# Kernel tuning notes

Hardware: AMD Instinct MI355X
Metric: run time of the kernel (lower is better)

Reference implementation:

```python
import jax, jax.numpy as jnp
import numpy as np

N, K, A, P, HID = 32768, 32, 4, 128, 256
RELMAX, NBINS, DMIN, DMAX = 32, 16, 0.0, 22.0
EPS = 1e-6


def _frames(pos):
    # Gram-Schmidt rigid frame from backbone atoms N(0), CA(1), C(2).
    v1 = pos[:, 2] - pos[:, 1]
    v2 = pos[:, 0] - pos[:, 1]
    e1 = v1 / (jnp.linalg.norm(v1, axis=-1, keepdims=True) + EPS)
    u2 = v2 - jnp.sum(v2 * e1, axis=-1, keepdims=True) * e1
    e2 = u2 / (jnp.linalg.norm(u2, axis=-1, keepdims=True) + EPS)
    e3 = jnp.cross(e1, e2)
    R = jnp.stack([e1, e2, e3], axis=-1)  # [N,3,3], columns are basis vectors
    t = pos[:, 1]                         # CA translation
    return R, t


def _rbf(d):
    centers = jnp.linspace(DMIN, DMAX, NBINS)
    sigma = (DMAX - DMIN) / NBINS
    return jnp.exp(-((d[..., None] - centers) ** 2) / (2.0 * sigma ** 2))


def setup_inputs() -> dict:
    key = jax.random.key(0)
    ks = jax.random.split(key, 12)
    g = lambda k, shape: jax.random.normal(k, shape) / jnp.sqrt(jnp.float32(shape[0]))
    return {
        "pos": jax.random.normal(ks[0], (N, A, 3)) * 3.0,
        "neighbours": jax.random.randint(ks[1], (N, K), 0, N),
        "resi": jnp.arange(N),
        "chain": jnp.zeros((N,), jnp.int32),
        "batch": jnp.zeros((N,), jnp.int32),
        "mask": jnp.ones((N,), jnp.float32),
        "W_rel": g(ks[2], (2 * RELMAX + 1, P)),
        "W_dist": g(ks[3], (NBINS, P)),
        "W_dir": g(ks[4], (3, P)),
        "W_rot": g(ks[5], (9, P)),
        "W_vec": g(ks[6], (A * 3, P)),
        "ln_scale": jnp.ones((P,), jnp.float32),
        "ln_bias": jnp.zeros((P,), jnp.float32),
        "W1": g(ks[7], (P, HID)),
        "b1": jnp.zeros((HID,), jnp.float32),
        "W2": g(ks[8], (HID, P)),
        "b2": jnp.zeros((P,), jnp.float32),
    }


def reference(pos, neighbours, resi, chain, batch, mask,
              W_rel, W_dist, W_dir, W_rot, W_vec,
              ln_scale, ln_bias, W1, b1, W2, b2):
    # pair mask: both residues valid and neighbour not padded
    pair_mask = mask[:, None] * mask[neighbours] * (neighbours != -1)

    # --- sequence relative position (one-hot, clipped, same chain/batch) ---
    same = ((chain[:, None] == chain[neighbours]) &
            (batch[:, None] == batch[neighbours]))
    rel = jnp.clip(resi[neighbours] - resi[:, None], -RELMAX, RELMAX) + RELMAX
    rel_oh = jax.nn.one_hot(rel, 2 * RELMAX + 1, dtype=pos.dtype) * same[..., None]
    pair = jnp.einsum("nkf,fp->nkp", rel_oh, W_rel)

    # --- distance features (CA-CA RBF) ---
    ca = pos[:, 1]                                      # [N,3]
    diff = ca[neighbours] - ca[:, None]                 # [N,K,3]
    d = jnp.sqrt(jnp.sum(diff * diff, axis=-1) + EPS)
    pair += jnp.einsum("nkf,fp->nkp", _rbf(d), W_dist)

    # --- direction features (unit vector in local frame of i) ---
    R, t = _frames(pos)
    unit = diff / (d[..., None] + EPS)
    local_dir = jnp.einsum("nab,nka->nkb", R, unit)     # R_i^T u
    pair += jnp.einsum("nkf,fp->nkp", local_dir, W_dir)

    # --- relative rotation features R_i^T R_j, flattened ---
    Rj = R[neighbours]                                  # [N,K,3,3]
    rel_rot = jnp.einsum("nab,nkac->nkbc", R, Rj).reshape(pos.shape[0], K, 9)
    pair += jnp.einsum("nkf,fp->nkp", rel_rot, W_rot)

    # --- pair vector features: neighbour atoms in frame of i ---
    vec = pos[neighbours] - t[:, None, None]            # [N,K,A,3]
    local_vec = jnp.einsum("nab,nkAa->nkAb", R, vec).reshape(pos.shape[0], K, A * 3)
    pair += jnp.einsum("nkf,fp->nkp", local_vec, W_vec)

    # --- LayerNorm over feature dim ---
    mu = jnp.mean(pair, axis=-1, keepdims=True)
    var = jnp.mean((pair - mu) ** 2, axis=-1, keepdims=True)
    pair = (pair - mu) / jnp.sqrt(var + 1e-5) * ln_scale + ln_bias

    # --- MLP (gelu, hidden = 2 * pair_size) ---
    h = jax.nn.gelu(jnp.einsum("nkp,ph->nkh", pair, W1) + b1)
    pair = jnp.einsum("nkh,hp->nkp", h, W2) + b2
    return pair, pair_mask


if __name__ == "__main__":
    out, pm = reference(**setup_inputs())
    print(out.shape, pm.shape)
```

## Files before the change

### kernel.cpp

```cpp
#include <hip/hip_runtime.h>
#include <hip/hip_bf16.h>

#define N_NODES 32768
#define NK      1048576

typedef __bf16 bf16x8 __attribute__((ext_vector_type(8)));
typedef float  f32x4  __attribute__((ext_vector_type(4)));
typedef short  short4v __attribute__((ext_vector_type(4)));
typedef int    int4v  __attribute__((ext_vector_type(4)));
typedef int    int2v  __attribute__((ext_vector_type(2)));

#define WAIT_LGKM() asm volatile("s_waitcnt lgkmcnt(0)" ::: "memory")

static __device__ __forceinline__ unsigned fbits(float f) {
    union { float f; unsigned u; } v; v.f = f; return v.u;
}
static __device__ __forceinline__ unsigned short f2bf(float f) {
    unsigned u = fbits(f);
    return (unsigned short)((u + 0x7fffu + ((u >> 16) & 1u)) >> 16);
}

static __device__ __forceinline__ void make_frame(const float* __restrict__ p, float* __restrict__ R) {
    float v1x = p[6]-p[3], v1y = p[7]-p[4], v1z = p[8]-p[5];
    float v2x = p[0]-p[3], v2y = p[1]-p[4], v2z = p[2]-p[5];
    float i1 = 1.f/(sqrtf(v1x*v1x+v1y*v1y+v1z*v1z)+1e-6f);
    float e1x=v1x*i1, e1y=v1y*i1, e1z=v1z*i1;
    float dt = v2x*e1x+v2y*e1y+v2z*e1z;
    float u2x=v2x-dt*e1x, u2y=v2y-dt*e1y, u2z=v2z-dt*e1z;
    float i2 = 1.f/(sqrtf(u2x*u2x+u2y*u2y+u2z*u2z)+1e-6f);
    float e2x=u2x*i2, e2y=u2y*i2, e2z=u2z*i2;
    float e3x = e1y*e2z - e1z*e2y;
    float e3y = e1z*e2x - e1x*e2z;
    float e3z = e1x*e2y - e1y*e2x;
    R[0]=e1x; R[1]=e2x; R[2]=e3x;
    R[3]=e1y; R[4]=e2y; R[5]=e3y;
    R[6]=e1z; R[7]=e2z; R[8]=e3z;
}

__global__ void sd_prep_weights(const float* __restrict__ W1, const float* __restrict__ W2,
                                const float* __restrict__ Wd, const float* __restrict__ Wdir,
                                const float* __restrict__ Wrot, const float* __restrict__ Wvec,
                                unsigned short* __restrict__ wftp, unsigned short* __restrict__ w1p,
                                unsigned short* __restrict__ w2p) {
    int i = blockIdx.x*256 + threadIdx.x;
    if (i < 8192) {
        int fragid = i >> 9, lane = (i >> 3) & 63, j = i & 7;
        int pb = fragid >> 1, ks = fragid & 1;
        int f = 8*(lane>>4) + j + 32*ks;
        int p = pb*16 + (lane & 15);
        float v = 0.f;
        if (f < 16)       v = Wd[f*128+p];
        else if (f < 19)  v = Wdir[(f-16)*128+p];
        else if (f < 28)  v = Wrot[(f-19)*128+p];
        else if (f < 40)  v = Wvec[(f-28)*128+p];
        wftp[i] = f2bf(v);
    } else if (i < 40960) {
        int idx = i - 8192;
        int fragid = idx >> 9, lane = (idx >> 3) & 63, j = idx & 7;
        int ht = fragid >> 2, ks = fragid & 3;
        int h = ht*16 + (lane & 15);
        int p = 8*(lane>>4) + j + 32*ks;
        w1p[idx] = f2bf(W1[p*256 + h]);
    } else if (i < 73728) {
        int idx = i - 40960;
        int fragid = idx >> 9, lane = (idx >> 3) & 63, j = idx & 7;
        int pt = fragid >> 3, ktp = fragid & 7;
        int half = j >> 2, jj = j & 3;
        int h = (2*ktp + half)*16 + 4*(lane>>4) + jj;
        int p = pt*16 + (lane & 15);
        w2p[idx] = f2bf(W2[h*128 + p]);
    }
}

__global__ void sd_mask_kernel(const int* __restrict__ nbr, const float* __restrict__ mask,
                               float* __restrict__ outm) {
    int g = blockIdx.x*256 + threadIdx.x;
    if (g >= NK) return;
    int j = nbr[g];
    int n = g >> 5;
    float pm = mask[n] * mask[j & (N_NODES-1)] * ((j != -1) ? 1.f : 0.f);
    outm[g] = pm;
}

#define MFMA32(a,b,c) __builtin_amdgcn_mfma_f32_16x16x32_bf16((a),(b),(c),0,0,0)
#define MFMA16(a,b,c) __builtin_amdgcn_mfma_f32_16x16x16bf16_1k((a),(b),(c),0,0,0)

__global__ __launch_bounds__(256, 3) void sd_fused_kernel(
    const float* __restrict__ pos, const int* __restrict__ nbr,
    const int* __restrict__ resi, const int* __restrict__ chain,
    const int* __restrict__ batch, const float* __restrict__ W_rel,
    const float* __restrict__ ln_scale, const float* __restrict__ ln_bias,
    const float* __restrict__ b1, const float* __restrict__ b2,
    const char* __restrict__ wftp_c, const char* __restrict__ w1p_c,
    const char* __restrict__ w2p_c,
    float* __restrict__ out)
{
    __shared__ __align__(16) char smem[49664];
    const int t    = threadIdx.x;
    const int lane = t & 63;
    const int wid  = t >> 6;
    const int lrow = lane & 15;
    const int lk   = lane >> 4;
    const int edge0 = blockIdx.x * 128 + wid * 32;
    char* Fv = smem + wid * 12288;
    char* Xv = Fv + 4096;
    int* meta = (int*)(smem + 49152 + wid*128);

    {
        int4v z = (int4v){0,0,0,0};
        #pragma unroll
        for (int k = 0; k < 4; ++k) *(int4v*)(Fv + lane*64 + k*16) = z;
    }
    WAIT_LGKM();

    {
        const int e   = lane >> 1;
        const int sub = lane & 1;
        const int g   = edge0 + e;
        const int n   = g >> 5;
        const int jn  = nbr[g] & (N_NODES - 1);
        float pn[12], pj[12];
        #pragma unroll
        for (int r = 0; r < 3; ++r) {
            f32x4 a = *(const f32x4*)(pos + n*12 + r*4);
            f32x4 b = *(const f32x4*)(pos + jn*12 + r*4);
            #pragma unroll
            for (int c = 0; c < 4; ++c) { pn[r*4+c] = a[c]; pj[r*4+c] = b[c]; }
        }
        float Rn[9], Rj[9];
        make_frame(pn, Rn); make_frame(pj, Rj);
        float dx = pj[3]-pn[3], dy = pj[4]-pn[4], dz = pj[5]-pn[5];
        float d = sqrtf(dx*dx + dy*dy + dz*dz + 1e-6f);
        float inv = 1.f/(d + 1e-6f);
        float ux = dx*inv, uy = dy*inv, uz = dz*inv;
        float feats[40];
        #pragma unroll
        for (int bb = 0; bb < 16; ++bb) {
            float ee = d - (22.f/15.f)*bb;
            feats[bb] = __expf(-ee*ee*0.264462809917f);
        }
        #pragma unroll
        for (int bb = 0; bb < 3; ++bb)
            feats[16+bb] = Rn[bb]*ux + Rn[3+bb]*uy + Rn[6+bb]*uz;
        #pragma unroll
        for (int bb = 0; bb < 3; ++bb)
            #pragma unroll
            for (int cc = 0; cc < 3; ++cc)
                feats[19+bb*3+cc] = Rn[bb]*Rj[cc] + Rn[3+bb]*Rj[3+cc] + Rn[6+bb]*Rj[6+cc];
        #pragma unroll
        for (int aa = 0; aa < 4; ++aa) {
            float vx = pj[aa*3+0]-pn[3], vy = pj[aa*3+1]-pn[4], vz = pj[aa*3+2]-pn[5];
            #pragma unroll
            for (int bb = 0; bb < 3; ++bb)
                feats[28+aa*3+bb] = Rn[bb]*vx + Rn[3+bb]*vy + Rn[6+bb]*vz;
        }
        char* fb = Fv + e*128;
        const int rx = (e & 7) << 4;
        if (!sub) {
            #pragma unroll
            for (int f = 0; f < 20; ++f)
                *(unsigned short*)(fb + ((2*f) ^ rx)) = f2bf(feats[f]);
        } else {
            #pragma unroll
            for (int f = 20; f < 40; ++f)
                *(unsigned short*)(fb + ((2*f) ^ rx)) = f2bf(feats[f]);
            int same = (chain[n]==chain[jn]) & (batch[n]==batch[jn]);
            int rel = resi[jn] - resi[n];
            rel = (rel < -32 ? -32 : (rel > 32 ? 32 : rel)) + 32;
            meta[e] = same ? (rel + 1) : 0;
        }
    }
    WAIT_LGKM();

    const int rxl = (lrow & 7) << 4;

    f32x4 accF[2][8];
    #pragma unroll
    for (int ni = 0; ni < 2; ++ni)
        #pragma unroll
        for (int pb = 0; pb < 8; ++pb) accF[ni][pb] = (f32x4){0.f,0.f,0.f,0.f};
    #pragma unroll
    for (int ks = 0; ks < 2; ++ks) {
        bf16x8 a0 = *(const bf16x8*)(Fv + lrow*128       + ((16*lk + 64*ks) ^ rxl));
        bf16x8 a1 = *(const bf16x8*)(Fv + (16+lrow)*128  + ((16*lk + 64*ks) ^ rxl));
        #pragma unroll
        for (int pb = 0; pb < 8; ++pb) {
            bf16x8 b = *(const bf16x8*)(wftp_c + ((pb*2 + ks)*64 + lane)*16);
            accF[0][pb] = MFMA32(a0, b, accF[0][pb]);
            accF[1][pb] = MFMA32(a1, b, accF[1][pb]);
        }
    }

    {
        float lnSv[8], lnBv[8];
        #pragma unroll
        for (int pb = 0; pb < 8; ++pb) {
            lnSv[pb] = ln_scale[pb*16 + lrow];
            lnBv[pb] = ln_bias [pb*16 + lrow];
        }
        #pragma unroll
        for (int ni = 0; ni < 2; ++ni) {
            #pragma unroll
            for (int i = 0; i < 4; ++i) {
                int er = ni*16 + 4*lk + i;
                int mt = meta[er];
                const float* wrel = W_rel + (mt > 0 ? (mt-1)*128 : 0);
                float sv = (mt > 0) ? 1.f : 0.f;
                float s = 0.f, ss = 0.f;
                #pragma unroll
                for (int pb = 0; pb < 8; ++pb) {
                    float x = accF[ni][pb][i] + sv * wrel[pb*16 + lrow];
                    accF[ni][pb][i] = x;
                    s += x; ss += x*x;
                }
                s  += __shfl_xor(s,1);  s  += __shfl_xor(s,2);  s  += __shfl_xor(s,4);  s  += __shfl_xor(s,8);
                ss += __shfl_xor(ss,1); ss += __shfl_xor(ss,2); ss += __shfl_xor(ss,4); ss += __shfl_xor(ss,8);
                float mu  = s * 0.0078125f;
                float var = ss * 0.0078125f - mu*mu;
                float rstd = rsqrtf(var + 1e-5f);
                char* xb = Xv + er*256;
                const int rx2 = (er & 7) << 4;
                #pragma unroll
                for (int pb = 0; pb < 8; ++pb) {
                    float xv = (accF[ni][pb][i] - mu) * rstd * lnSv[pb] + lnBv[pb];
                    *(unsigned short*)(xb + ((2*(pb*16 + lrow)) ^ rx2)) = f2bf(xv);
                }
            }
        }
    }
    WAIT_LGKM();

    bf16x8 bx[2][4];
    #pragma unroll
    for (int ni = 0; ni < 2; ++ni)
        #pragma unroll
        for (int ks = 0; ks < 4; ++ks)
            bx[ni][ks] = *(const bf16x8*)(Xv + (ni*16+lrow)*256 + ((16*lk + 64*ks) ^ rxl));

    f32x4 acc2[2][8];
    #pragma unroll
    for (int ni = 0; ni < 2; ++ni)
        #pragma unroll
        for (int pt = 0; pt < 8; ++pt) acc2[ni][pt] = (f32x4){0.f,0.f,0.f,0.f};

    const float C2 = -2.30220797f;
    #pragma unroll
    for (int hc = 0; hc < 8; ++hc) {
        f32x4 acc1[2][2];
        #pragma unroll
        for (int m = 0; m < 2; ++m)
            #pragma unroll
            for (int ni = 0; ni < 2; ++ni) acc1[m][ni] = (f32x4){0.f,0.f,0.f,0.f};
        #pragma unroll
        for (int ks = 0; ks < 4; ++ks) {
            bf16x8 a0 = *(const bf16x8*)(w1p_c + (((hc*2  )*4 + ks)*64 + lane)*16);
            bf16x8 a1 = *(const bf16x8*)(w1p_c + (((hc*2+1)*4 + ks)*64 + lane)*16);
            acc1[0][0] = MFMA32(a0, bx[0][ks], acc1[0][0]);
            acc1[0][1] = MFMA32(a0, bx[1][ks], acc1[0][1]);
            acc1[1][0] = MFMA32(a1, bx[0][ks], acc1[1][0]);
            acc1[1][1] = MFMA32(a1, bx[1][ks], acc1[1][1]);
        }
        f32x4 b1v[2];
        b1v[0] = *(const f32x4*)(b1 + hc*32      + 4*lk);
        b1v[1] = *(const f32x4*)(b1 + hc*32 + 16 + 4*lk);
        short4v pa[2][2];
        #pragma unroll
        for (int m = 0; m < 2; ++m) {
            #pragma unroll
            for (int ni = 0; ni < 2; ++ni) {
                #pragma unroll
                for (int i = 0; i < 4; ++i) {
                    float x  = acc1[m][ni][i] + b1v[m][i];
                    float tt = x * __builtin_fmaf(0.044715f, x*x, 1.0f);
                    float ex = __builtin_amdgcn_exp2f(C2 * tt);
                    pa[m][ni][i] = (short)f2bf(x / (1.0f + ex));
                }
            }
        }
        #pragma unroll
        for (int pt = 0; pt < 8; ++pt) {
            int4v w = *(const int4v*)(w2p_c + ((pt*8 + hc)*64 + lane)*16);
            short4v f0 = __builtin_bit_cast(short4v, (int2v){w[0], w[1]});
            short4v f1 = __builtin_bit_cast(short4v, (int2v){w[2], w[3]});
            acc2[0][pt] = MFMA16(pa[0][0], f0, acc2[0][pt]);
            acc2[1][pt] = MFMA16(pa[0][1], f0, acc2[1][pt]);
            acc2[0][pt] = MFMA16(pa[1][0], f1, acc2[0][pt]);
            acc2[1][pt] = MFMA16(pa[1][1], f1, acc2[1][pt]);
        }
    }

    float b2v[8];
    #pragma unroll
    for (int pt = 0; pt < 8; ++pt) b2v[pt] = b2[pt*16 + lrow];
    #pragma unroll
    for (int ni = 0; ni < 2; ++ni) {
        #pragma unroll
        for (int pt = 0; pt < 8; ++pt) {
            #pragma unroll
            for (int i = 0; i < 4; ++i) {
                int er = ni*16 + 4*lk + i;
                out[(size_t)(edge0 + er)*128 + pt*16 + lrow] = acc2[ni][pt][i] + b2v[pt];
            }
        }
    }
}

extern "C" void kernel_launch(void* const* d_in, const int* in_sizes, int n_in,
                              void* d_out, int out_size, void* d_ws, size_t ws_size,
                              hipStream_t stream) {
    const float* pos      = (const float*)d_in[0];
    const int*   nbr      = (const int*)d_in[1];
    const int*   resi     = (const int*)d_in[2];
    const int*   chain    = (const int*)d_in[3];
    const int*   batch    = (const int*)d_in[4];
    const float* mask     = (const float*)d_in[5];
    const float* W_rel    = (const float*)d_in[6];
    const float* W_dist   = (const float*)d_in[7];
    const float* W_dir    = (const float*)d_in[8];
    const float* W_rot    = (const float*)d_in[9];
    const float* W_vec    = (const float*)d_in[10];
    const float* ln_scale = (const float*)d_in[11];
    const float* ln_bias  = (const float*)d_in[12];
    const float* W1       = (const float*)d_in[13];
    const float* b1       = (const float*)d_in[14];
    const float* W2       = (const float*)d_in[15];
    const float* b2       = (const float*)d_in[16];

    unsigned short* wftp = (unsigned short*)d_ws;
    unsigned short* w1p  = wftp + 8192;
    unsigned short* w2p  = w1p + 32768;
    float* out  = (float*)d_out;
    float* outm = out + (size_t)NK * 128;

    sd_prep_weights<<<288, 256, 0, stream>>>(W1, W2, W_dist, W_dir, W_rot, W_vec,
                                             wftp, w1p, w2p);
    sd_mask_kernel<<<NK/256, 256, 0, stream>>>(nbr, mask, outm);
    sd_fused_kernel<<<NK/128, 256, 0, stream>>>(pos, nbr, resi, chain, batch, W_rel,
                                                ln_scale, ln_bias, b1, b2,
                                                (const char*)wftp, (const char*)w1p,
                                                (const char*)w2p, out);
}
```

Before: 450.7 us.

## Use K=32 MFMA for second GEMM, hardware bf16 convert, DPP row reductions

The second MLP GEMM now packs the GELU outputs into 8-wide bf16 fragments and issues 16x16x32 MFMAs instead of pairs of 16x16x16 ones, which halves the MFMA instruction count. The packed W2 layout is adjusted to match. Software round-to-nearest bf16 conversion is replaced with the hardware conversion intrinsic, and the LayerNorm 16-lane reductions use DPP adds instead of shuffles. This cuts instruction and LDS-permute overhead, but correctness depends on the new fragment k-ordering matching the repacked W2.

```diff
diff --git a/kernel.cpp b/kernel.cpp
--- a/kernel.cpp
+++ b/kernel.cpp
@@ -6,9 +6,8 @@
 
 typedef __bf16 bf16x8 __attribute__((ext_vector_type(8)));
 typedef float  f32x4  __attribute__((ext_vector_type(4)));
-typedef short  short4v __attribute__((ext_vector_type(4)));
+typedef short  short8v __attribute__((ext_vector_type(8)));
 typedef int    int4v  __attribute__((ext_vector_type(4)));
-typedef int    int2v  __attribute__((ext_vector_type(2)));
 
 #define WAIT_LGKM() asm volatile("s_waitcnt lgkmcnt(0)" ::: "memory")
 
@@ -18,6 +17,22 @@
 static __device__ __forceinline__ unsigned short f2bf(float f) {
     unsigned u = fbits(f);
     return (unsigned short)((u + 0x7fffu + ((u >> 16) & 1u)) >> 16);
+}
+static __device__ __forceinline__ unsigned short hwbf(float f) {
+    return __builtin_bit_cast(unsigned short, __float2bfloat16(f));
+}
+
+template<int CTRL>
+static __device__ __forceinline__ float dpp_add(float v) {
+    int sw = __builtin_amdgcn_update_dpp(0, __builtin_bit_cast(int, v), CTRL, 0xf, 0xf, true);
+    return v + __builtin_bit_cast(float, sw);
+}
+static __device__ __forceinline__ float row16_sum(float v) {
+    v = dpp_add<0xB1>(v);
+    v = dpp_add<0x4E>(v);
+    v = dpp_add<0x141>(v);
+    v = dpp_add<0x140>(v);
+    return v;
 }
 
 static __device__ __forceinline__ void make_frame(const float* __restrict__ p, float* __restrict__ R) {
@@ -64,9 +79,8 @@
     } else if (i < 73728) {
         int idx = i - 40960;
         int fragid = idx >> 9, lane = (idx >> 3) & 63, j = idx & 7;
-        int pt = fragid >> 3, ktp = fragid & 7;
-        int half = j >> 2, jj = j & 3;
-        int h = (2*ktp + half)*16 + 4*(lane>>4) + jj;
+        int pt = fragid >> 3, hc = fragid & 7;
+        int h = hc*32 + (j>>2)*16 + 4*(lane>>4) + (j&3);
         int p = pt*16 + (lane & 15);
         w2p[idx] = f2bf(W2[h*128 + p]);
     }
@@ -83,7 +97,6 @@
 }
 
 #define MFMA32(a,b,c) __builtin_amdgcn_mfma_f32_16x16x32_bf16((a),(b),(c),0,0,0)
-#define MFMA16(a,b,c) __builtin_amdgcn_mfma_f32_16x16x16bf16_1k((a),(b),(c),0,0,0)
 
 __global__ __launch_bounds__(256, 3) void sd_fused_kernel(
     const float* __restrict__ pos, const int* __restrict__ nbr,
@@ -159,11 +172,11 @@
         if (!sub) {
             #pragma unroll
             for (int f = 0; f < 20; ++f)
-                *(unsigned short*)(fb + ((2*f) ^ rx)) = f2bf(feats[f]);
+                *(unsigned short*)(fb + ((2*f) ^ rx)) = hwbf(feats[f]);
         } else {
             #pragma unroll
             for (int f = 20; f < 40; ++f)
-                *(unsigned short*)(fb + ((2*f) ^ rx)) = f2bf(feats[f]);
+                *(unsigned short*)(fb + ((2*f) ^ rx)) = hwbf(feats[f]);
             int same = (chain[n]==chain[jn]) & (batch[n]==batch[jn]);
             int rel = resi[jn] - resi[n];
             rel = (rel < -32 ? -32 : (rel > 32 ? 32 : rel)) + 32;
@@ -213,8 +226,8 @@
                     accF[ni][pb][i] = x;
                     s += x; ss += x*x;
                 }
-                s  += __shfl_xor(s,1);  s  += __shfl_xor(s,2);  s  += __shfl_xor(s,4);  s  += __shfl_xor(s,8);
-                ss += __shfl_xor(ss,1); ss += __shfl_xor(ss,2); ss += __shfl_xor(ss,4); ss += __shfl_xor(ss,8);
+                s  = row16_sum(s);
+                ss = row16_sum(ss);
                 float mu  = s * 0.0078125f;
                 float var = ss * 0.0078125f - mu*mu;
                 float rstd = rsqrtf(var + 1e-5f);
@@ -223,7 +236,7 @@
                 #pragma unroll
                 for (int pb = 0; pb < 8; ++pb) {
                     float xv = (accF[ni][pb][i] - mu) * rstd * lnSv[pb] + lnBv[pb];
-                    *(unsigned short*)(xb + ((2*(pb*16 + lrow)) ^ rx2)) = f2bf(xv);
+                    *(unsigned short*)(xb + ((2*(pb*16 + lrow)) ^ rx2)) = hwbf(xv);
                 }
             }
         }
@@ -263,7 +276,7 @@
         f32x4 b1v[2];
         b1v[0] = *(const f32x4*)(b1 + hc*32      + 4*lk);
         b1v[1] = *(const f32x4*)(b1 + hc*32 + 16 + 4*lk);
-        short4v pa[2][2];
+        short8v ga[2];
         #pragma unroll
         for (int m = 0; m < 2; ++m) {
             #pragma unroll
@@ -273,19 +286,17 @@
                     float x  = acc1[m][ni][i] + b1v[m][i];
                     float tt = x * __builtin_fmaf(0.044715f, x*x, 1.0f);
                     float ex = __builtin_amdgcn_exp2f(C2 * tt);
-                    pa[m][ni][i] = (short)f2bf(x / (1.0f + ex));
+                    ga[ni][m*4+i] = (short)hwbf(x / (1.0f + ex));
                 }
             }
         }
+        bf16x8 ga0 = __builtin_bit_cast(bf16x8, ga[0]);
+        bf16x8 ga1 = __builtin_bit_cast(bf16x8, ga[1]);
         #pragma unroll
         for (int pt = 0; pt < 8; ++pt) {
-            int4v w = *(const int4v*)(w2p_c + ((pt*8 + hc)*64 + lane)*16);
-            short4v f0 = __builtin_bit_cast(short4v, (int2v){w[0], w[1]});
-            short4v f1 = __builtin_bit_cast(short4v, (int2v){w[2], w[3]});
-            acc2[0][pt] = MFMA16(pa[0][0], f0, acc2[0][pt]);
-            acc2[1][pt] = MFMA16(pa[0][1], f0, acc2[1][pt]);
-            acc2[0][pt] = MFMA16(pa[1][0], f1, acc2[0][pt]);
-            acc2[1][pt] = MFMA16(pa[1][1], f1, acc2[1][pt]);
+            bf16x8 wf = *(const bf16x8*)(w2p_c + ((pt*8 + hc)*64 + lane)*16);
+            acc2[0][pt] = MFMA32(ga0, wf, acc2[0][pt]);
+            acc2[1][pt] = MFMA32(ga1, wf, acc2[1][pt]);
         }
     }
 
```

Measured after the change: 393.1 us. -12.8%, faster.
